# Kernel tuning notes

Hardware: AMD Instinct MI355X
Metric: run time of the kernel (lower is better)

Reference implementation:

```python
import jax, jax.numpy as jnp
import numpy as np

N = 50000       # nodes
E = 1_600_000   # edges (avg degree 32)
NFEAT = 256
NHID = 128
NCLASS = 128    # must equal NHID for the gated skip connection to type-check


def setup_inputs() -> dict:
    key = jax.random.key(0)
    ks = jax.random.split(key, 16)
    g = 0.02  # xavier gain used in the module
    inp = {
        "x": jax.random.normal(ks[0], (N, NFEAT), dtype=jnp.float32),
        "row": jax.random.randint(ks[1], (E,), 0, N, dtype=jnp.int32),
        "col": jax.random.randint(ks[2], (E,), 0, N, dtype=jnp.int32),
        # GatedSkipConnection params (shared across the three skip calls)
        "W_sc": jax.random.normal(ks[3], (NFEAT, NHID), dtype=jnp.float32) * 0.05,
        "W_ci": jax.random.normal(ks[4], (NHID, NHID), dtype=jnp.float32) * 0.05,
        "b_ci": jnp.zeros((NHID,), dtype=jnp.float32),
        "W_co": jax.random.normal(ks[5], (NHID, NHID), dtype=jnp.float32) * 0.05,
        "b_co": jnp.zeros((NHID,), dtype=jnp.float32),
        # GraphSAGE layer weights: [2*in, out], bias [1, out] (init to 0 per module)
        "W0": jax.random.normal(ks[6], (2 * NFEAT, NHID), dtype=jnp.float32) * g,
        "b0": jnp.zeros((1, NHID), dtype=jnp.float32),
        "W1": jax.random.normal(ks[7], (2 * NHID, NHID), dtype=jnp.float32) * g,
        "b1": jnp.zeros((1, NHID), dtype=jnp.float32),
        "W2": jax.random.normal(ks[8], (2 * NHID, NCLASS), dtype=jnp.float32) * g,
        "b2": jnp.zeros((1, NCLASS), dtype=jnp.float32),
        # fc0: Linear(nhid, nclass)
        "Wf": jax.random.normal(ks[9], (NHID, NCLASS), dtype=jnp.float32) * 0.05,
        "bf": jnp.zeros((NCLASS,), dtype=jnp.float32),
    }
    return inp


def _sage(x, row, col, inv_deg, W, b):
    # adj @ x : sum source features x[col] into destination rows `row`
    agg = jax.ops.segment_sum(x[col], row, num_segments=N)  # [N, d]
    agg = agg * inv_deg[:, None]                            # degree normalization
    support = jnp.concatenate([x, agg], axis=1)             # [N, 2d]
    return support @ W + b


def _gsc(in_x, out_x, W_sc, W_ci, b_ci, W_co, b_co):
    in_x = in_x @ W_sc if in_x.shape[1] != out_x.shape[1] else in_x
    z = jax.nn.sigmoid(in_x @ W_ci + b_ci + out_x @ W_co + b_co)
    return z * out_x + (1.0 - z) * in_x


def reference(x, row, col, W_sc, W_ci, b_ci, W_co, b_co,
              W0, b0, W1, b1, W2, b2, Wf, bf):
    deg = jax.ops.segment_sum(jnp.ones((E,), x.dtype), row, num_segments=N)
    inv_deg = 1.0 / jnp.maximum(deg, 1.0)  # guard isolated nodes

    residual = x
    o1 = _sage(x, row, col, inv_deg, W0, b0)
    o3 = jax.nn.relu(_gsc(residual, o1, W_sc, W_ci, b_ci, W_co, b_co))
    o4 = _sage(o3, row, col, inv_deg, W1, b1)
    o6 = jax.nn.relu(_gsc(residual, o4, W_sc, W_ci, b_ci, W_co, b_co))
    o7 = _sage(o6, row, col, inv_deg, W2, b2)
    o8 = _gsc(residual, o7, W_sc, W_ci, b_ci, W_co, b_co)
    return o8 @ Wf + bf
```

## Files before the change

### kernel.cpp

```cpp
#include <hip/hip_runtime.h>
#include <hip/hip_bf16.h>
#include <hip/hip_fp16.h>
#include <math.h>

#define NN 50000
#define EE 1600000
#define NFEAT 256
#define NHID 128
#define RNG 6250
#define NPASS 8
#define CPAD 16

typedef _Float16 f16;
typedef _Float16 f16x8 __attribute__((ext_vector_type(8)));
typedef _Float16 f16x4 __attribute__((ext_vector_type(4)));
typedef float f32x4 __attribute__((ext_vector_type(4)));

struct WPtrs {
    const float* s[10];
    f16* d[10];
};

__global__ __launch_bounds__(256) void k_prep(const float* __restrict__ x,
                                              f16* __restrict__ xh, int n4,
                                              int* __restrict__ cnt, int nz4,
                                              WPtrs wp, int wtotal,
                                              int zb0, int wb0, int wblocks) {
    int b = blockIdx.x;
    if (b < zb0) {
        int i = b * 256 + threadIdx.x;
        if (i < n4) {
            float4 v = reinterpret_cast<const float4*>(x)[i];
            f16x4 h = {(f16)v.x, (f16)v.y, (f16)v.z, (f16)v.w};
            reinterpret_cast<f16x4*>(xh)[i] = h;
        }
    } else if (b < wb0) {
        int i = (b - zb0) * 256 + threadIdx.x;
        if (i < nz4) reinterpret_cast<int4*>(cnt)[i] = make_int4(0, 0, 0, 0);
    } else {
        for (int idx = (b - wb0) * 256 + threadIdx.x; idx < wtotal;
             idx += wblocks * 256) {
            int wsel, rem, K;
            if (idx < 3 * 32768) { wsel = idx >> 15; rem = idx & 32767; K = 256; }
            else { int t = idx - 3 * 32768; wsel = 3 + (t >> 14); rem = t & 16383; K = 128; }
            int k = rem >> 7, c = rem & 127;
            wp.d[wsel][c * K + k] = (f16)wp.s[wsel][rem];
        }
    }
}

__global__ void k_slot(const int* __restrict__ row, int* __restrict__ cnt,
                       int* __restrict__ eslot, int e) {
    int i = blockIdx.x * 256 + threadIdx.x;
    if (i < e) eslot[i] = atomicAdd(&cnt[(size_t)row[i] * CPAD], 1);
}

__global__ void k_scan1(const int* __restrict__ cnt, int* __restrict__ bsum, int n) {
    __shared__ int s[256];
    int t = threadIdx.x;
    int i = blockIdx.x * 256 + t;
    s[t] = (i < n) ? cnt[(size_t)i * CPAD] : 0;
    __syncthreads();
    for (int off = 128; off > 0; off >>= 1) {
        if (t < off) s[t] += s[t + off];
        __syncthreads();
    }
    if (t == 0) bsum[blockIdx.x] = s[0];
}

__global__ void k_scan3(const int* __restrict__ cnt, const int* __restrict__ bsum,
                        int* __restrict__ rp, float* __restrict__ invd,
                        int n, int nb) {
    __shared__ int buf[2][256];
    __shared__ int bpre[2][256];
    int t = threadIdx.x;

    bpre[0][t] = (t < nb) ? bsum[t] : 0;
    __syncthreads();
    int bs = 0;
    for (int off = 1; off < 256; off <<= 1) {
        int v = bpre[bs][t];
        if (t >= off) v += bpre[bs][t - off];
        bpre[bs ^ 1][t] = v;
        bs ^= 1;
        __syncthreads();
    }
    int base = (blockIdx.x == 0) ? 0 : bpre[bs][blockIdx.x - 1];

    int i = blockIdx.x * 256 + t;
    int v = (i < n) ? cnt[(size_t)i * CPAD] : 0;
    buf[0][t] = v;
    __syncthreads();
    int sel = 0;
    for (int off = 1; off < 256; off <<= 1) {
        int x = buf[sel][t];
        if (t >= off) x += buf[sel][t - off];
        buf[sel ^ 1][t] = x;
        sel ^= 1;
        __syncthreads();
    }
    int incl = buf[sel][t];
    int excl = incl - v;
    if (i < n) {
        rp[i] = base + excl;
        invd[i] = 1.0f / fmaxf((float)v, 1.0f);
        if (i == n - 1) rp[n] = base + incl;
    }
}

__global__ void k_fill8(const int* __restrict__ row, const int* __restrict__ col,
                        const int* __restrict__ eslot, const int* __restrict__ rp,
                        int* __restrict__ ci, int e) {
    int i = blockIdx.x * 256 + threadIdx.x;
    if (i >= e) return;
    int r = row[i];
    int lo = blockIdx.y * RNG;
    if (r >= lo && r < lo + RNG) ci[rp[r] + eslot[i]] = col[i];
}

__global__ __launch_bounds__(256) void k_agg2h(const f16* __restrict__ P,
                                               const int* __restrict__ rp,
                                               const int* __restrict__ ci,
                                               const float* __restrict__ invd,
                                               const f16* __restrict__ T,
                                               f16* __restrict__ OUT, int n) {
    int node = blockIdx.x * 16 + (threadIdx.x >> 4);
    if (node >= n) return;
    int lane = threadIdx.x & 15;
    int s = rp[node], e = rp[node + 1];
    float acc[8];
#pragma unroll
    for (int q = 0; q < 8; ++q) acc[q] = 0.0f;
    int j = s;
    for (; j + 8 <= e; j += 8) {
        f16x8 v[8];
#pragma unroll
        for (int u = 0; u < 8; ++u)
            v[u] = *reinterpret_cast<const f16x8*>(P + (size_t)ci[j + u] * 128 + lane * 8);
#pragma unroll
        for (int q = 0; q < 8; ++q)
            acc[q] += (((float)v[0][q] + (float)v[1][q]) + ((float)v[2][q] + (float)v[3][q])) +
                      (((float)v[4][q] + (float)v[5][q]) + ((float)v[6][q] + (float)v[7][q]));
    }
    for (; j < e; ++j) {
        f16x8 v0 = *reinterpret_cast<const f16x8*>(P + (size_t)ci[j] * 128 + lane * 8);
#pragma unroll
        for (int q = 0; q < 8; ++q) acc[q] += (float)v0[q];
    }
    float scl = invd[node];
    f16x8 tv = *reinterpret_cast<const f16x8*>(T + (size_t)node * 128 + lane * 8);
    f16x8 o;
#pragma unroll
    for (int q = 0; q < 8; ++q) o[q] = (f16)((float)tv[q] + scl * acc[q]);
    *reinterpret_cast<f16x8*>(OUT + (size_t)node * 128 + lane * 8) = o;
}

#define LDSSTR 40

__device__ __forceinline__ void stage_A(const f16* __restrict__ A, f16* sA,
                                        int row0, int K, int kb, int tid, int n) {
    int r = tid >> 2, ch = tid & 3;
    int gr = row0 + r;
    uint4 v = make_uint4(0, 0, 0, 0);
    if (gr < n) v = *reinterpret_cast<const uint4*>(A + (size_t)gr * K + kb + ch * 8);
    *reinterpret_cast<uint4*>(sA + r * LDSSTR + ch * 8) = v;
}

__device__ __forceinline__ void stage_B(const f16* __restrict__ Wt, f16* sB,
                                        int K, int kb, int tid) {
#pragma unroll
    for (int i = 0; i < 2; ++i) {
        int idx = tid + i * 256;
        int c = idx >> 2, ch = idx & 3;
        uint4 v = *reinterpret_cast<const uint4*>(Wt + (size_t)c * K + kb + ch * 8);
        *reinterpret_cast<uint4*>(sB + c * LDSSTR + ch * 8) = v;
    }
}

template <int K, int NW, bool F32OUT>
__global__ __launch_bounds__(256) void k_mgemm(const f16* __restrict__ A,
                                               const f16* __restrict__ Wt0,
                                               const f16* __restrict__ Wt1,
                                               const f16* __restrict__ Wt2,
                                               const float* __restrict__ bias0,
                                               void* __restrict__ C0,
                                               void* __restrict__ C1,
                                               void* __restrict__ C2, int n) {
    __shared__ f16 sA[64 * LDSSTR];
    __shared__ f16 sB[128 * LDSSTR];

    const f16* Wt = Wt0;
    const float* bias = bias0;
    void* C = C0;
    if (NW > 1 && blockIdx.y == 1) { Wt = Wt1; bias = nullptr; C = C1; }
    if (NW > 2 && blockIdx.y == 2) { Wt = Wt2; bias = nullptr; C = C2; }

    const int tid = threadIdx.x;
    const int row0 = blockIdx.x * 64;
    const int wid = tid >> 6, l = tid & 63;
    const int wr = wid >> 1, wc = wid & 1;
    const int lr = l & 15, lk = (l >> 4) * 8;

    f32x4 acc[2][4];
#pragma unroll
    for (int m = 0; m < 2; ++m)
#pragma unroll
        for (int q = 0; q < 4; ++q) acc[m][q] = (f32x4){0.f, 0.f, 0.f, 0.f};

    for (int kt = 0; kt < K / 32; ++kt) {
        stage_A(A, sA, row0, K, kt * 32, tid, n);
        stage_B(Wt, sB, K, kt * 32, tid);
        __syncthreads();
        f16x8 aF[2], bF[4];
#pragma unroll
        for (int m = 0; m < 2; ++m)
            aF[m] = *reinterpret_cast<f16x8*>(sA + (wr * 32 + m * 16 + lr) * LDSSTR + lk);
#pragma unroll
        for (int q = 0; q < 4; ++q)
            bF[q] = *reinterpret_cast<f16x8*>(sB + (wc * 64 + q * 16 + lr) * LDSSTR + lk);
#pragma unroll
        for (int m = 0; m < 2; ++m)
#pragma unroll
            for (int q = 0; q < 4; ++q)
                acc[m][q] = __builtin_amdgcn_mfma_f32_16x16x32_f16(aF[m], bF[q],
                                                                   acc[m][q], 0, 0, 0);
        __syncthreads();
    }

    const int lr4 = (l >> 4) * 4;
#pragma unroll
    for (int m = 0; m < 2; ++m)
#pragma unroll
        for (int q = 0; q < 4; ++q) {
            int c = wc * 64 + q * 16 + (l & 15);
            float b = bias ? bias[c] : 0.0f;
#pragma unroll
            for (int reg = 0; reg < 4; ++reg) {
                int r = row0 + wr * 32 + m * 16 + lr4 + reg;
                if (r >= n) continue;
                float v = acc[m][q][reg] + b;
                if (F32OUT) ((float*)C)[(size_t)r * 128 + c] = v;
                else        ((f16*)C)[(size_t)r * 128 + c] = (f16)v;
            }
        }
}

template <int RELU>
__global__ __launch_bounds__(256) void k_ggemm(const f16* __restrict__ Asc,
                                               const f16* __restrict__ At0,
                                               const f16* __restrict__ Wci,
                                               const f16* __restrict__ Wco,
                                               const float* __restrict__ bci,
                                               const float* __restrict__ bco,
                                               f16* __restrict__ C, int n) {
    __shared__ f16 sA[64 * LDSSTR];
    __shared__ f16 sB[128 * LDSSTR];

    const int tid = threadIdx.x;
    const int row0 = blockIdx.x * 64;
    const int wid = tid >> 6, l = tid & 63;
    const int wr = wid >> 1, wc = wid & 1;
    const int lr = l & 15, lk = (l >> 4) * 8;

    f32x4 acc[2][4];
#pragma unroll
    for (int m = 0; m < 2; ++m)
#pragma unroll
        for (int q = 0; q < 4; ++q) acc[m][q] = (f32x4){0.f, 0.f, 0.f, 0.f};

    for (int kt = 0; kt < 8; ++kt) {
        const f16* A = (kt < 4) ? Asc : At0;
        const f16* Wt = (kt < 4) ? Wci : Wco;
        int kb = (kt & 3) * 32;
        stage_A(A, sA, row0, 128, kb, tid, n);
        stage_B(Wt, sB, 128, kb, tid);
        __syncthreads();
        f16x8 aF[2], bF[4];
#pragma unroll
        for (int m = 0; m < 2; ++m)
            aF[m] = *reinterpret_cast<f16x8*>(sA + (wr * 32 + m * 16 + lr) * LDSSTR + lk);
#pragma unroll
        for (int q = 0; q < 4; ++q)
            bF[q] = *reinterpret_cast<f16x8*>(sB + (wc * 64 + q * 16 + lr) * LDSSTR + lk);
#pragma unroll
        for (int m = 0; m < 2; ++m)
#pragma unroll
            for (int q = 0; q < 4; ++q)
                acc[m][q] = __builtin_amdgcn_mfma_f32_16x16x32_f16(aF[m], bF[q],
                                                                   acc[m][q], 0, 0, 0);
        __syncthreads();
    }

    const int lr4 = (l >> 4) * 4;
#pragma unroll
    for (int m = 0; m < 2; ++m)
#pragma unroll
        for (int q = 0; q < 4; ++q) {
            int c = wc * 64 + q * 16 + (l & 15);
            float b = bci[c] + bco[c];
#pragma unroll
            for (int reg = 0; reg < 4; ++reg) {
                int r = row0 + wr * 32 + m * 16 + lr4 + reg;
                if (r >= n) continue;
                float v = acc[m][q][reg] + b;
                float z = 1.0f / (1.0f + __expf(-v));
                float o = (float)At0[(size_t)r * 128 + c];
                float s = (float)Asc[(size_t)r * 128 + c];
                float outv = z * o + (1.0f - z) * s;
                if (RELU) outv = fmaxf(outv, 0.0f);
                C[(size_t)r * 128 + c] = (f16)outv;
            }
        }
}

extern "C" void kernel_launch(void* const* d_in, const int* in_sizes, int n_in,
                              void* d_out, int out_size, void* d_ws, size_t ws_size,
                              hipStream_t stream) {
    const float* x    = (const float*)d_in[0];
    const int*   row  = (const int*)d_in[1];
    const int*   col  = (const int*)d_in[2];
    const float* W_sc = (const float*)d_in[3];
    const float* W_ci = (const float*)d_in[4];
    const float* b_ci = (const float*)d_in[5];
    const float* W_co = (const float*)d_in[6];
    const float* b_co = (const float*)d_in[7];
    const float* W0   = (const float*)d_in[8];
    const float* b0   = (const float*)d_in[9];
    const float* W1   = (const float*)d_in[10];
    const float* b1   = (const float*)d_in[11];
    const float* W2   = (const float*)d_in[12];
    const float* b2   = (const float*)d_in[13];
    const float* Wf   = (const float*)d_in[14];
    const float* bf   = (const float*)d_in[15];
    float* out = (float*)d_out;

    char* p = (char*)d_ws;
    auto alloc = [&](size_t bytes) {
        char* q = p;
        p += (bytes + 255) & ~(size_t)255;
        return q;
    };
    int*   cnt   = (int*)alloc((size_t)NN * CPAD * 4);
    int*   rp    = (int*)alloc((NN + 1) * 4);
    int*   bsum  = (int*)alloc(256 * 4);
    float* invd  = (float*)alloc(NN * 4);
    int*   ci    = (int*)alloc(EE * 4);
    int*   eslot = (int*)alloc(EE * 4);
    f16*   x_h   = (f16*)alloc((size_t)NN * 256 * 2);
    f16*   sc_h  = (f16*)alloc((size_t)NN * 128 * 2);
    f16*   T_h   = (f16*)alloc((size_t)NN * 128 * 2);
    f16*   P_h   = (f16*)alloc((size_t)NN * 128 * 2);
    f16*   t0_h  = (f16*)alloc((size_t)NN * 128 * 2);
    f16*   t1_h  = (f16*)alloc((size_t)NN * 128 * 2);
    f16* W0t_t = (f16*)alloc(256 * 128 * 2);
    f16* W0b_t = (f16*)alloc(256 * 128 * 2);
    f16* Wsc_t = (f16*)alloc(256 * 128 * 2);
    f16* W1t_t = (f16*)alloc(128 * 128 * 2);
    f16* W1b_t = (f16*)alloc(128 * 128 * 2);
    f16* W2t_t = (f16*)alloc(128 * 128 * 2);
    f16* W2b_t = (f16*)alloc(128 * 128 * 2);
    f16* Wci_t = (f16*)alloc(128 * 128 * 2);
    f16* Wco_t = (f16*)alloc(128 * 128 * 2);
    f16* Wf_t  = (f16*)alloc(128 * 128 * 2);

    const int NB_N  = (NN + 255) / 256;
    const int NB_E  = (EE + 255) / 256;
    const int GB    = (NN + 63) / 64;
    const int AGG_B = (NN + 15) / 16;

    const int N4   = NN * 256 / 4;
    const int NZ4  = NN * CPAD / 4;
    const int ZB0  = (N4 + 255) / 256;
    const int WB0  = ZB0 + (NZ4 + 255) / 256;
    const int WBLK = 84;
    const int WTOT = 3 * 32768 + 7 * 16384;
    WPtrs wp;
    wp.s[0] = W0;             wp.d[0] = W0t_t;
    wp.s[1] = W0 + 256 * 128; wp.d[1] = W0b_t;
    wp.s[2] = W_sc;           wp.d[2] = Wsc_t;
    wp.s[3] = W1;             wp.d[3] = W1t_t;
    wp.s[4] = W1 + 128 * 128; wp.d[4] = W1b_t;
    wp.s[5] = W2;             wp.d[5] = W2t_t;
    wp.s[6] = W2 + 128 * 128; wp.d[6] = W2b_t;
    wp.s[7] = W_ci;           wp.d[7] = Wci_t;
    wp.s[8] = W_co;           wp.d[8] = Wco_t;
    wp.s[9] = Wf;             wp.d[9] = Wf_t;
    k_prep<<<WB0 + WBLK, 256, 0, stream>>>(x, x_h, N4, cnt, NZ4, wp, WTOT,
                                           ZB0, WB0, WBLK);

    k_slot<<<NB_E, 256, 0, stream>>>(row, cnt, eslot, EE);
    k_scan1<<<NB_N, 256, 0, stream>>>(cnt, bsum, NN);
    k_scan3<<<NB_N, 256, 0, stream>>>(cnt, bsum, rp, invd, NN, NB_N);
    k_fill8<<<dim3(NB_E, NPASS), 256, 0, stream>>>(row, col, eslot, rp, ci, EE);

    k_mgemm<256, 3, false><<<dim3(GB, 3), 256, 0, stream>>>(
        x_h, W0t_t, W0b_t, Wsc_t, b0, T_h, P_h, sc_h, NN);
    k_agg2h<<<AGG_B, 256, 0, stream>>>(P_h, rp, ci, invd, T_h, t0_h, NN);
    k_ggemm<1><<<GB, 256, 0, stream>>>(sc_h, t0_h, Wci_t, Wco_t,
                                       b_ci, b_co, t1_h, NN);

    k_mgemm<128, 2, false><<<dim3(GB, 2), 256, 0, stream>>>(
        t1_h, W1t_t, W1b_t, nullptr, b1, T_h, P_h, nullptr, NN);
    k_agg2h<<<AGG_B, 256, 0, stream>>>(P_h, rp, ci, invd, T_h, t0_h, NN);
    k_ggemm<1><<<GB, 256, 0, stream>>>(sc_h, t0_h, Wci_t, Wco_t,
                                       b_ci, b_co, t1_h, NN);

    k_mgemm<128, 2, false><<<dim3(GB, 2), 256, 0, stream>>>(
        t1_h, W2t_t, W2b_t, nullptr, b2, T_h, P_h, nullptr, NN);
    k_agg2h<<<AGG_B, 256, 0, stream>>>(P_h, rp, ci, invd, T_h, t0_h, NN);
    k_ggemm<0><<<GB, 256, 0, stream>>>(sc_h, t0_h, Wci_t, Wco_t,
                                       b_ci, b_co, t1_h, NN);

    k_mgemm<128, 1, true><<<GB, 256, 0, stream>>>(
        t1_h, Wf_t, nullptr, nullptr, bf, out, nullptr, nullptr, NN);
}
```

Measured before the change: 541.8 us.

## Double-buffer GEMM tiles at 128 rows, pack edge slot with row, halve fill passes

The dense GEMM kernels now take 128-row tiles with a 4x4 MFMA accumulator per wave and double-buffered LDS. Each next k-tile is prefetched into registers while the current tile runs through MFMA, which is meant to hide global-load latency and improve weight reuse. The CSR build packs the per-edge slot and the destination row into a single int, so the fill kernel reads one array instead of two, and the fill now runs in 4 row-range passes instead of 8. The packing assumes row fits in 16 bits and slot in 15, which holds for these sizes. The larger tiles also use more registers and LDS per block and launch fewer blocks.

Measured after the change: 566.0 us. +4.5%, slower.

```diff
diff --git a/kernel.cpp b/kernel.cpp
--- a/kernel.cpp
+++ b/kernel.cpp
@@ -7,13 +7,12 @@
 #define EE 1600000
 #define NFEAT 256
 #define NHID 128
-#define RNG 6250
-#define NPASS 8
+#define RNG 12500
+#define NPASS 4
 #define CPAD 16
 
 typedef _Float16 f16;
 typedef _Float16 f16x8 __attribute__((ext_vector_type(8)));
-typedef _Float16 f16x4 __attribute__((ext_vector_type(4)));
 typedef float f32x4 __attribute__((ext_vector_type(4)));
 
 struct WPtrs {
@@ -31,8 +30,9 @@
         int i = b * 256 + threadIdx.x;
         if (i < n4) {
             float4 v = reinterpret_cast<const float4*>(x)[i];
-            f16x4 h = {(f16)v.x, (f16)v.y, (f16)v.z, (f16)v.w};
-            reinterpret_cast<f16x4*>(xh)[i] = h;
+            f16 h0 = (f16)v.x, h1 = (f16)v.y, h2 = (f16)v.z, h3 = (f16)v.w;
+            f16* d = xh + (size_t)i * 4;
+            d[0] = h0; d[1] = h1; d[2] = h2; d[3] = h3;
         }
     } else if (b < wb0) {
         int i = (b - zb0) * 256 + threadIdx.x;
@@ -50,9 +50,13 @@
 }
 
 __global__ void k_slot(const int* __restrict__ row, int* __restrict__ cnt,
-                       int* __restrict__ eslot, int e) {
+                       int* __restrict__ epack, int e) {
     int i = blockIdx.x * 256 + threadIdx.x;
-    if (i < e) eslot[i] = atomicAdd(&cnt[(size_t)row[i] * CPAD], 1);
+    if (i < e) {
+        int r = row[i];
+        int s = atomicAdd(&cnt[(size_t)r * CPAD], 1);
+        epack[i] = (s << 16) | r;
+    }
 }
 
 __global__ void k_scan1(const int* __restrict__ cnt, int* __restrict__ bsum, int n) {
@@ -108,14 +112,14 @@
     }
 }
 
-__global__ void k_fill8(const int* __restrict__ row, const int* __restrict__ col,
-                        const int* __restrict__ eslot, const int* __restrict__ rp,
-                        int* __restrict__ ci, int e) {
+__global__ void k_fill(const int* __restrict__ epack, const int* __restrict__ col,
+                       const int* __restrict__ rp, int* __restrict__ ci, int e) {
     int i = blockIdx.x * 256 + threadIdx.x;
     if (i >= e) return;
-    int r = row[i];
+    int pk = epack[i];
+    int r = pk & 0xFFFF;
     int lo = blockIdx.y * RNG;
-    if (r >= lo && r < lo + RNG) ci[rp[r] + eslot[i]] = col[i];
+    if (r >= lo && r < lo + RNG) ci[rp[r] + (pk >> 16)] = col[i];
 }
 
 __global__ __launch_bounds__(256) void k_agg2h(const f16* __restrict__ P,
@@ -156,38 +160,66 @@
 }
 
 #define LDSSTR 40
-
-__device__ __forceinline__ void stage_A(const f16* __restrict__ A, f16* sA,
-                                        int row0, int K, int kb, int tid, int n) {
-    int r = tid >> 2, ch = tid & 3;
-    int gr = row0 + r;
-    uint4 v = make_uint4(0, 0, 0, 0);
-    if (gr < n) v = *reinterpret_cast<const uint4*>(A + (size_t)gr * K + kb + ch * 8);
-    *reinterpret_cast<uint4*>(sA + r * LDSSTR + ch * 8) = v;
-}
-
-__device__ __forceinline__ void stage_B(const f16* __restrict__ Wt, f16* sB,
-                                        int K, int kb, int tid) {
+#define LBUF (128 * LDSSTR)
+
+struct Stage { uint4 a[2], b[2]; };
+
+__device__ __forceinline__ void ld_tile(Stage& s, const f16* __restrict__ A,
+                                        const f16* __restrict__ Wt, int row0,
+                                        int K, int kb, int tid, int n) {
 #pragma unroll
     for (int i = 0; i < 2; ++i) {
         int idx = tid + i * 256;
-        int c = idx >> 2, ch = idx & 3;
-        uint4 v = *reinterpret_cast<const uint4*>(Wt + (size_t)c * K + kb + ch * 8);
-        *reinterpret_cast<uint4*>(sB + c * LDSSTR + ch * 8) = v;
-    }
+        int r = idx >> 2, ch = idx & 3;
+        int gr = row0 + r;
+        s.a[i] = (gr < n)
+            ? *reinterpret_cast<const uint4*>(A + (size_t)gr * K + kb + ch * 8)
+            : make_uint4(0, 0, 0, 0);
+        s.b[i] = *reinterpret_cast<const uint4*>(Wt + (size_t)r * K + kb + ch * 8);
+    }
+}
+
+__device__ __forceinline__ void st_tile(const Stage& s, f16* __restrict__ sA,
+                                        f16* __restrict__ sB, int tid) {
+#pragma unroll
+    for (int i = 0; i < 2; ++i) {
+        int idx = tid + i * 256;
+        int r = idx >> 2, ch = idx & 3;
+        *reinterpret_cast<uint4*>(sA + r * LDSSTR + ch * 8) = s.a[i];
+        *reinterpret_cast<uint4*>(sB + r * LDSSTR + ch * 8) = s.b[i];
+    }
+}
+
+__device__ __forceinline__ void mfma_tile(const f16* __restrict__ sA,
+                                          const f16* __restrict__ sB,
+                                          f32x4 acc[4][4], int wr, int wc,
+                                          int lr, int lk) {
+    f16x8 aF[4], bF[4];
+#pragma unroll
+    for (int m = 0; m < 4; ++m)
+        aF[m] = *reinterpret_cast<const f16x8*>(sA + (wr * 64 + m * 16 + lr) * LDSSTR + lk);
+#pragma unroll
+    for (int q = 0; q < 4; ++q)
+        bF[q] = *reinterpret_cast<const f16x8*>(sB + (wc * 64 + q * 16 + lr) * LDSSTR + lk);
+#pragma unroll
+    for (int m = 0; m < 4; ++m)
+#pragma unroll
+        for (int q = 0; q < 4; ++q)
+            acc[m][q] = __builtin_amdgcn_mfma_f32_16x16x32_f16(aF[m], bF[q],
+                                                               acc[m][q], 0, 0, 0);
 }
 
 template <int K, int NW, bool F32OUT>
-__global__ __launch_bounds__(256) void k_mgemm(const f16* __restrict__ A,
-                                               const f16* __restrict__ Wt0,
-                                               const f16* __restrict__ Wt1,
-                                               const f16* __restrict__ Wt2,
-                                               const float* __restrict__ bias0,
-                                               void* __restrict__ C0,
-                                               void* __restrict__ C1,
-                                               void* __restrict__ C2, int n) {
-    __shared__ f16 sA[64 * LDSSTR];
-    __shared__ f16 sB[128 * LDSSTR];
+__global__ __launch_bounds__(256, 3) void k_mgemm(const f16* __restrict__ A,
+                                                  const f16* __restrict__ Wt0,
+                                                  const f16* __restrict__ Wt1,
+                                                  const f16* __restrict__ Wt2,
+                                                  const float* __restrict__ bias0,
+                                                  void* __restrict__ C0,
+                                                  void* __restrict__ C1,
+                                                  void* __restrict__ C2, int n) {
+    constexpr int NT = K / 32;
+    __shared__ f16 lds[2][2 * LBUF];
 
     const f16* Wt = Wt0;
     const float* bias = bias0;
@@ -196,47 +228,44 @@
     if (NW > 2 && blockIdx.y == 2) { Wt = Wt2; bias = nullptr; C = C2; }
 
     const int tid = threadIdx.x;
-    const int row0 = blockIdx.x * 64;
+    const int row0 = blockIdx.x * 128;
     const int wid = tid >> 6, l = tid & 63;
     const int wr = wid >> 1, wc = wid & 1;
     const int lr = l & 15, lk = (l >> 4) * 8;
 
-    f32x4 acc[2][4];
-#pragma unroll
-    for (int m = 0; m < 2; ++m)
+    f32x4 acc[4][4];
+#pragma unroll
+    for (int m = 0; m < 4; ++m)
 #pragma unroll
         for (int q = 0; q < 4; ++q) acc[m][q] = (f32x4){0.f, 0.f, 0.f, 0.f};
 
-    for (int kt = 0; kt < K / 32; ++kt) {
-        stage_A(A, sA, row0, K, kt * 32, tid, n);
-        stage_B(Wt, sB, K, kt * 32, tid);
-        __syncthreads();
-        f16x8 aF[2], bF[4];
-#pragma unroll
-        for (int m = 0; m < 2; ++m)
-            aF[m] = *reinterpret_cast<f16x8*>(sA + (wr * 32 + m * 16 + lr) * LDSSTR + lk);
-#pragma unroll
-        for (int q = 0; q < 4; ++q)
-            bF[q] = *reinterpret_cast<f16x8*>(sB + (wc * 64 + q * 16 + lr) * LDSSTR + lk);
-#pragma unroll
-        for (int m = 0; m < 2; ++m)
-#pragma unroll
-            for (int q = 0; q < 4; ++q)
-                acc[m][q] = __builtin_amdgcn_mfma_f32_16x16x32_f16(aF[m], bF[q],
-                                                                   acc[m][q], 0, 0, 0);
-        __syncthreads();
+    Stage s;
+    ld_tile(s, A, Wt, row0, K, 0, tid, n);
+    st_tile(s, lds[0], lds[0] + LBUF, tid);
+    __syncthreads();
+
+    int cur = 0;
+    for (int t = 0; t < NT; ++t) {
+        Stage nx;
+        if (t + 1 < NT) ld_tile(nx, A, Wt, row0, K, (t + 1) * 32, tid, n);
+        mfma_tile(lds[cur], lds[cur] + LBUF, acc, wr, wc, lr, lk);
+        if (t + 1 < NT) {
+            st_tile(nx, lds[cur ^ 1], lds[cur ^ 1] + LBUF, tid);
+            __syncthreads();
+            cur ^= 1;
+        }
     }
 
     const int lr4 = (l >> 4) * 4;
 #pragma unroll
-    for (int m = 0; m < 2; ++m)
+    for (int m = 0; m < 4; ++m)
 #pragma unroll
         for (int q = 0; q < 4; ++q) {
             int c = wc * 64 + q * 16 + (l & 15);
             float b = bias ? bias[c] : 0.0f;
 #pragma unroll
             for (int reg = 0; reg < 4; ++reg) {
-                int r = row0 + wr * 32 + m * 16 + lr4 + reg;
+                int r = row0 + wr * 64 + m * 16 + lr4 + reg;
                 if (r >= n) continue;
                 float v = acc[m][q][reg] + b;
                 if (F32OUT) ((float*)C)[(size_t)r * 128 + c] = v;
@@ -246,67 +275,66 @@
 }
 
 template <int RELU>
-__global__ __launch_bounds__(256) void k_ggemm(const f16* __restrict__ Asc,
-                                               const f16* __restrict__ At0,
-                                               const f16* __restrict__ Wci,
-                                               const f16* __restrict__ Wco,
-                                               const float* __restrict__ bci,
-                                               const float* __restrict__ bco,
-                                               f16* __restrict__ C, int n) {
-    __shared__ f16 sA[64 * LDSSTR];
-    __shared__ f16 sB[128 * LDSSTR];
+__global__ __launch_bounds__(256, 3) void k_ggemm(const f16* __restrict__ Asc,
+                                                  const f16* __restrict__ At0,
+                                                  const f16* __restrict__ Wci,
+                                                  const f16* __restrict__ Wco,
+                                                  const float* __restrict__ bci,
+                                                  const float* __restrict__ bco,
+                                                  f16* __restrict__ C, int n) {
+    constexpr int NT = 8;
+    __shared__ f16 lds[2][2 * LBUF];
 
     const int tid = threadIdx.x;
-    const int row0 = blockIdx.x * 64;
+    const int row0 = blockIdx.x * 128;
     const int wid = tid >> 6, l = tid & 63;
     const int wr = wid >> 1, wc = wid & 1;
     const int lr = l & 15, lk = (l >> 4) * 8;
 
-    f32x4 acc[2][4];
-#pragma unroll
-    for (int m = 0; m < 2; ++m)
+    f32x4 acc[4][4];
+#pragma unroll
+    for (int m = 0; m < 4; ++m)
 #pragma unroll
         for (int q = 0; q < 4; ++q) acc[m][q] = (f32x4){0.f, 0.f, 0.f, 0.f};
 
-    for (int kt = 0; kt < 8; ++kt) {
-        const f16* A = (kt < 4) ? Asc : At0;
-        const f16* Wt = (kt < 4) ? Wci : Wco;
-        int kb = (kt & 3) * 32;
-        stage_A(A, sA, row0, 128, kb, tid, n);
-        stage_B(Wt, sB, 128, kb, tid);
-        __syncthreads();
-        f16x8 aF[2], bF[4];
-#pragma unroll
-        for (int m = 0; m < 2; ++m)
-            aF[m] = *reinterpret_cast<f16x8*>(sA + (wr * 32 + m * 16 + lr) * LDSSTR + lk);
-#pragma unroll
-        for (int q = 0; q < 4; ++q)
-            bF[q] = *reinterpret_cast<f16x8*>(sB + (wc * 64 + q * 16 + lr) * LDSSTR + lk);
-#pragma unroll
-        for (int m = 0; m < 2; ++m)
-#pragma unroll
-            for (int q = 0; q < 4; ++q)
-                acc[m][q] = __builtin_amdgcn_mfma_f32_16x16x32_f16(aF[m], bF[q],
-                                                                   acc[m][q], 0, 0, 0);
-        __syncthreads();
+    Stage s;
+    ld_tile(s, Asc, Wci, row0, 128, 0, tid, n);
+    st_tile(s, lds[0], lds[0] + LBUF, tid);
+    __syncthreads();
+
+    int cur = 0;
+    for (int t = 0; t < NT; ++t) {
+        Stage nx;
+        if (t + 1 < NT) {
+            int tn = t + 1;
+            const f16* An = (tn < 4) ? Asc : At0;
+            const f16* Wn = (tn < 4) ? Wci : Wco;
+            ld_tile(nx, An, Wn, row0, 128, (tn & 3) * 32, tid, n);
+        }
+        mfma_tile(lds[cur], lds[cur] + LBUF, acc, wr, wc, lr, lk);
+        if (t + 1 < NT) {
+            st_tile(nx, lds[cur ^ 1], lds[cur ^ 1] + LBUF, tid);
+            __syncthreads();
+            cur ^= 1;
+        }
     }
 
     const int lr4 = (l >> 4) * 4;
 #pragma unroll
-    for (int m = 0; m < 2; ++m)
+    for (int m = 0; m < 4; ++m)
 #pragma unroll
         for (int q = 0; q < 4; ++q) {
             int c = wc * 64 + q * 16 + (l & 15);
             float b = bci[c] + bco[c];
 #pragma unroll
             for (int reg = 0; reg < 4; ++reg) {
-                int r = row0 + wr * 32 + m * 16 + lr4 + reg;
+                int r = row0 + wr * 64 + m * 16 + lr4 + reg;
                 if (r >= n) continue;
                 float v = acc[m][q][reg] + b;
                 float z = 1.0f / (1.0f + __expf(-v));
                 float o = (float)At0[(size_t)r * 128 + c];
-                float s = (float)Asc[(size_t)r * 128 + c];
-                float outv = z * o + (1.0f - z) * s;
+                float sv = (float)Asc[(size_t)r * 128 + c];
+                float outv = z * o + (1.0f - z) * sv;
                 if (RELU) outv = fmaxf(outv, 0.0f);
                 C[(size_t)r * 128 + c] = (f16)outv;
             }
@@ -345,7 +373,7 @@
     int*   bsum  = (int*)alloc(256 * 4);
     float* invd  = (float*)alloc(NN * 4);
     int*   ci    = (int*)alloc(EE * 4);
-    int*   eslot = (int*)alloc(EE * 4);
+    int*   epack = (int*)alloc(EE * 4);
     f16*   x_h   = (f16*)alloc((size_t)NN * 256 * 2);
     f16*   sc_h  = (f16*)alloc((size_t)NN * 128 * 2);
     f16*   T_h   = (f16*)alloc((size_t)NN * 128 * 2);
@@ -365,7 +393,7 @@
 
     const int NB_N  = (NN + 255) / 256;
     const int NB_E  = (EE + 255) / 256;
-    const int GB    = (NN + 63) / 64;
+    const int GB    = (NN + 127) / 128;
     const int AGG_B = (NN + 15) / 16;
 
     const int N4   = NN * 256 / 4;
@@ -388,10 +416,10 @@
     k_prep<<<WB0 + WBLK, 256, 0, stream>>>(x, x_h, N4, cnt, NZ4, wp, WTOT,
                                            ZB0, WB0, WBLK);
 
-    k_slot<<<NB_E, 256, 0, stream>>>(row, cnt, eslot, EE);
+    k_slot<<<NB_E, 256, 0, stream>>>(row, cnt, epack, EE);
     k_scan1<<<NB_N, 256, 0, stream>>>(cnt, bsum, NN);
     k_scan3<<<NB_N, 256, 0, stream>>>(cnt, bsum, rp, invd, NN, NB_N);
-    k_fill8<<<dim3(NB_E, NPASS), 256, 0, stream>>>(row, col, eslot, rp, ci, EE);
+    k_fill<<<dim3(NB_E, NPASS), 256, 0, stream>>>(epack, col, rp, ci, EE);
 
     k_mgemm<256, 3, false><<<dim3(GB, 3), 256, 0, stream>>>(
         x_h, W0t_t, W0b_t, Wsc_t, b0, T_h, P_h, sc_h, NN);
```
